# Performance work log

Hardware: AMD Instinct MI355X
Metric: run time of the kernel (lower is better)

Reference implementation:

```python
import jax, jax.numpy as jnp
import numpy as np

D_MODEL = 1024
SCALE = 1.0 / np.sqrt(D_MODEL).astype(np.float32)


def setup_inputs() -> dict:
    key = jax.random.key(0)
    ks = jax.random.split(key, 9)
    B, S, D = 4, 2048, D_MODEL
    init = 1.0 / np.sqrt(D).astype(np.float32)
    return {
        "q": jax.random.normal(ks[0], (B, S, D), jnp.float32),
        "k": jax.random.normal(ks[1], (B, S, D), jnp.float32),
        "v": jax.random.normal(ks[2], (B, S, D), jnp.float32),
        "Wq": jax.random.uniform(ks[3], (D, D), jnp.float32, -init, init),
        "bq": jax.random.uniform(ks[4], (D,), jnp.float32, -init, init),
        "Wk": jax.random.uniform(ks[5], (D, D), jnp.float32, -init, init),
        "bk": jax.random.uniform(ks[6], (D,), jnp.float32, -init, init),
        "Wv": jax.random.uniform(ks[7], (D, D), jnp.float32, -init, init),
        "bv": jax.random.uniform(ks[8], (D,), jnp.float32, -init, init),
    }


def reference(q, k, v, Wq, bq, Wk, bk, Wv, bv):
    # Linear projections (torch Linear: x @ W.T + b)
    qp = jnp.einsum('bsd,ed->bse', q, Wq) + bq
    kp = jnp.einsum('bsd,ed->bse', k, Wk) + bk
    vp = jnp.einsum('bsd,ed->bse', v, Wv) + bv
    qp = jax.nn.softmax(qp, axis=-1)          # softmax over feature dim
    kp = jax.nn.softmax(kp, axis=-2) * SCALE  # softmax over sequence dim
    vp = jax.nn.softmax(vp, axis=-2)          # softmax over sequence dim
    attn_weights = jnp.einsum('bqd,bkd->bqk', qp, kp)  # [B,S,S]
    output = jnp.einsum('bqk,bkd->bqd', attn_weights, vp)
    return (output, attn_weights)
```

## Files before the change

### kernel.cpp

```cpp
#include <hip/hip_runtime.h>
#include <math.h>


typedef float  f32x4  __attribute__((ext_vector_type(4)));
typedef __bf16 bf16x8 __attribute__((ext_vector_type(8)));
typedef int    i32x4  __attribute__((ext_vector_type(4)));
typedef unsigned short u16;

__device__ __forceinline__ float b2f(u16 u) {
    unsigned int i = ((unsigned int)u) << 16; float f;
    __builtin_memcpy(&f, &i, 4); return f;
}
__device__ __forceinline__ u16 f2b(float f) {
    unsigned int i; __builtin_memcpy(&i, &f, 4);
    i += 0x7FFFu + ((i >> 16) & 1u);
    return (u16)(i >> 16);
}

__global__ __launch_bounds__(256) void cvt_all(
    const float4* __restrict__ q, const float4* __restrict__ k,
    const float4* __restrict__ v, const float4* __restrict__ Wq,
    const float4* __restrict__ Wk, const float4* __restrict__ Wv,
    const float* __restrict__ bq, const float* __restrict__ bk,
    const float* __restrict__ bv,
    ushort4* __restrict__ qb, ushort4* __restrict__ kb,
    ushort4* __restrict__ vb, ushort4* __restrict__ Wb,
    float* __restrict__ biasCat)
{
    int bid = blockIdx.x, t = threadIdx.x;
    const float4* s; ushort4* d; int idx;
    if (bid < 8192)       { s = q;  d = qb;            idx = bid * 256 + t; }
    else if (bid < 16384) { s = k;  d = kb;            idx = (bid - 8192) * 256 + t; }
    else if (bid < 24576) { s = v;  d = vb;            idx = (bid - 16384) * 256 + t; }
    else if (bid < 25600) { s = Wq; d = Wb;            idx = (bid - 24576) * 256 + t; }
    else if (bid < 26624) { s = Wk; d = Wb + 262144;   idx = (bid - 25600) * 256 + t; }
    else if (bid < 27648) { s = Wv; d = Wb + 524288;   idx = (bid - 26624) * 256 + t; }
    else {
        for (int i = t; i < 3072; i += 256)
            biasCat[i] = (i < 1024) ? bq[i] : (i < 2048) ? bk[i - 1024] : bv[i - 2048];
        return;
    }
    float4 vv = s[idx];
    ushort4 o;
    o.x = f2b(vv.x); o.y = f2b(vv.y); o.z = f2b(vv.z); o.w = f2b(vv.w);
    d[idx] = o;
}

__global__ __launch_bounds__(512, 2) void gemm256_attn(
    const u16* __restrict__ Ap, const u16* __restrict__ Bp,
    float* __restrict__ C32, u16* __restrict__ C16,
    int N, int K, long long sA, long long sB, long long sC)
{
    __shared__ __align__(16) u16 lds[65536];

    const int tid  = threadIdx.x;
    const int lane = tid & 63;
    const int w    = tid >> 6;
    const int wr   = w >> 2, wc = w & 3;

    const int gx  = gridDim.x;
    const int tot = gx * gridDim.y;
    const int lin = blockIdx.y * gx + blockIdx.x;
    const int vlin = (lin & 7) * (tot >> 3) + (lin >> 3);
    const int bx = vlin % gx, by = vlin / gx;
    const int m0 = by * 256, n0 = bx * 256;
    const int z  = blockIdx.z;

    const u16* Ag = Ap + (size_t)z * sA;
    const u16* Bg = Bp + (size_t)z * sB;

    const int cl = tid ^ ((tid >> 4) & 6);
    const int lr = cl >> 3;
    const int ce = (cl & 7) * 8;
    const int arow = m0 + lr;
    const int brow = n0 + (lr & 31) + ((lr & 32) << 1);

    const int axr = ((lane >> 2) & 3) << 4;
    const int ar0 = (wr * 64 + (lane & 15)) * 64 + (lane >> 4) * 8;
    const int br0 = (wc * 32 + (lane & 15)) * 64 + (lane >> 4) * 8;

#define GLL16(gsrc, ldsoff)                                                    \
    __builtin_amdgcn_global_load_lds(                                          \
        (__attribute__((address_space(1))) void*)(uintptr_t)(gsrc),            \
        (__attribute__((address_space(3))) void*)&lds[ldsoff], 16, 0, 0)

#define STAGE_A(c, h, T)                                                       \
    do { const u16* _s = Ag + (size_t)(arow + (h) * 64) * K + (T) * 64 + ce;   \
         int _d = (((c) << 1) + (h)) * 8192 + tid * 8;                         \
         GLL16(_s, _d); GLL16(_s + (size_t)128 * K, _d + 4096); } while (0)

#define STAGE_B(c, g, T)                                                       \
    do { const u16* _s = Bg + (size_t)(brow + (g) * 32) * K + (T) * 64 + ce;   \
         int _d = 32768 + (((c) << 1) + (g)) * 8192 + tid * 8;                 \
         GLL16(_s, _d); GLL16(_s + (size_t)128 * K, _d + 4096); } while (0)

#define SBAR asm volatile("s_barrier" ::: "memory")

#define LDA(base)                                                              \
    _Pragma("unroll") for (int mi2 = 0; mi2 < 4; ++mi2)                        \
    _Pragma("unroll") for (int ks = 0; ks < 2; ++ks)                           \
        afr[mi2][ks] = __builtin_bit_cast(bf16x8,                              \
            *(const i32x4*)&lds[(base) + ((ar0 + mi2 * 1024 + ks * 32) ^ axr)]);

#define LDB(dst, base)                                                         \
    _Pragma("unroll") for (int ni2 = 0; ni2 < 2; ++ni2)                        \
    _Pragma("unroll") for (int ks = 0; ks < 2; ++ks)                           \
        dst[ni2][ks] = __builtin_bit_cast(bf16x8,                              \
            *(const i32x4*)&lds[(base) + ((br0 + ni2 * 1024 + ks * 32) ^ axr)]);

#define MFMA_Q(mb, nb, bfrag)                                                  \
    __builtin_amdgcn_s_setprio(1);                                             \
    _Pragma("unroll") for (int mi2 = 0; mi2 < 4; ++mi2)                        \
    _Pragma("unroll") for (int ni2 = 0; ni2 < 2; ++ni2)                        \
    _Pragma("unroll") for (int ks = 0; ks < 2; ++ks)                           \
        acc[(mb) + mi2][(nb) + ni2] = __builtin_amdgcn_mfma_f32_16x16x32_bf16( \
            afr[mi2][ks], bfrag[ni2][ks], acc[(mb) + mi2][(nb) + ni2], 0, 0, 0); \
    __builtin_amdgcn_s_setprio(0)

    f32x4 acc[8][4];
#pragma unroll
    for (int i = 0; i < 8; ++i)
#pragma unroll
        for (int j = 0; j < 4; ++j) acc[i][j] = (f32x4)0.0f;

    bf16x8 afr[4][2], b0f[2][2], b1f[2][2];

    const int nt = K >> 6;

    STAGE_A(0, 0, 0); STAGE_B(0, 0, 0);
    STAGE_A(0, 1, 0); STAGE_B(0, 1, 0);
    STAGE_A(1, 0, 1); STAGE_B(1, 0, 1);

    for (int T = 0; T < nt; ++T) {
        const int cur = T & 1, nxt = cur ^ 1;
        const int ab = (cur << 1) * 8192;
        const int bb = 32768 + (cur << 1) * 8192;

        if (T + 1 < nt) asm volatile("s_waitcnt vmcnt(4)" ::: "memory");
        else            asm volatile("s_waitcnt vmcnt(0)" ::: "memory");
        SBAR;
        LDA(ab); LDB(b0f, bb);
        if (T + 1 < nt) STAGE_B(nxt, 1, T + 1);
        SBAR;
        MFMA_Q(0, 0, b0f);
        SBAR;
        LDB(b1f, bb + 8192);
        if (T + 1 < nt) STAGE_A(nxt, 1, T + 1);
        SBAR;
        MFMA_Q(0, 2, b1f);
        SBAR;
        LDA(ab + 8192);
        if (T + 2 < nt) STAGE_A(cur, 0, T + 2);
        SBAR;
        MFMA_Q(4, 0, b0f);
        SBAR;
        if (T + 2 < nt) STAGE_B(cur, 0, T + 2);
        SBAR;
        MFMA_Q(4, 2, b1f);
        SBAR;
    }

    const int cr0 = m0 + wr * 128 + ((lane >> 4) << 2);
    const int cc0 = n0 + wc * 64 + (lane & 15);
    float* Cg = C32 + (size_t)z * sC;
#pragma unroll
    for (int mi = 0; mi < 8; ++mi)
#pragma unroll
        for (int ni = 0; ni < 4; ++ni)
#pragma unroll
            for (int j = 0; j < 4; ++j)
                Cg[(size_t)(cr0 + mi * 16 + j) * N + cc0 + ni * 16] = acc[mi][ni][j];

    u16* sE = lds;
    u16* Cb = C16 + (size_t)z * sC;
    const int wrow0 = ((lane >> 4) << 2);
    const int wcol0 = wc * 64 + (lane & 15);
    const int rr = tid >> 2;
    const int c0 = (tid & 3) * 8;
    __syncthreads();
#pragma unroll
    for (int p = 0; p < 2; ++p) {
        if (wr == p) {
#pragma unroll
            for (int mi = 0; mi < 8; ++mi)
#pragma unroll
                for (int ni = 0; ni < 4; ++ni)
#pragma unroll
                    for (int j = 0; j < 4; ++j)
                        sE[(wrow0 + mi * 16 + j) * 264 + wcol0 + ni * 16] =
                            f2b(acc[mi][ni][j]);
        }
        __syncthreads();
#pragma unroll
        for (int i = 0; i < 8; ++i) {
            i32x4 vv = *(const i32x4*)&sE[rr * 264 + c0 + i * 32];
            *(i32x4*)&Cb[(size_t)(m0 + p * 128 + rr) * N + n0 + c0 + i * 32] = vv;
        }
        if (p == 0) __syncthreads();
    }
#undef GLL16
#undef STAGE_A
#undef STAGE_B
#undef SBAR
#undef LDA
#undef LDB
#undef MFMA_Q
}

template<int EPI, int BM>
__global__ __launch_bounds__(256, BM == 128 ? 3 : 2) void gemm_bw(
    const u16* __restrict__ Ap, const u16* __restrict__ Bp,
    float* __restrict__ C32, u16* __restrict__ C16, u16* __restrict__ Calt,
    const float* __restrict__ bias, const float* __restrict__ vinv,
    int N, int K, long long sA, long long sB, long long sC)
{
    constexpr int AMI = BM / 32;
    constexpr int ALD = BM / 64;
    constexpr int ASZ = BM * 32;
    constexpr int BUF = ASZ + 4096;
    __shared__ __align__(16) u16 lds[3 * BUF];

    const int tid  = threadIdx.x;
    const int lane = tid & 63;
    const int w    = tid >> 6;
    const int wr   = w >> 1, wc = w & 1;

    const int gx  = gridDim.x;
    const int tot = gx * gridDim.y;
    const int lin = blockIdx.y * gx + blockIdx.x;
    const int vlin = (lin & 7) * (tot >> 3) + (lin >> 3);
    const int bx = vlin % gx, by = vlin / gx;
    const int m0 = by * BM, n0 = bx * 128;
    const int z  = blockIdx.z;

    const u16* Ag = Ap + (size_t)z * sA;
    const u16* Bg = Bp + (size_t)z * sB;

    const int cltid = tid ^ ((tid >> 3) & 3);
    const int crow  = cltid >> 2;
    const int ce    = (cltid & 3) * 8;

    const int exr = ((lane >> 1) & 3) << 3;
    const int ar0 = (wr * (BM / 2) + (lane & 15)) * 32 + (lane >> 4) * 8;
    const int br0 = (wc * 64 + (lane & 15)) * 32 + (lane >> 4) * 8;

#define GLLW(gsrc, ldsoff)                                                     \
    __builtin_amdgcn_global_load_lds(                                          \
        (__attribute__((address_space(1))) void*)(uintptr_t)(gsrc),            \
        (__attribute__((address_space(3))) void*)&lds[ldsoff], 16, 0, 0)

#define STAGE(buf, T)                                                          \
    do {                                                                       \
        _Pragma("unroll") for (int ld = 0; ld < ALD; ++ld)                     \
            GLLW(Ag + (size_t)(m0 + ld * 64 + crow) * K + (T) * 32 + ce,       \
                 (buf) + ld * 2048 + tid * 8);                                 \
        _Pragma("unroll") for (int ld = 0; ld < 2; ++ld)                       \
            GLLW(Bg + (size_t)(n0 + ld * 64 + crow) * K + (T) * 32 + ce,       \
                 (buf) + ASZ + ld * 2048 + tid * 8);                           \
    } while (0)

    f32x4 acc[AMI][4];
#pragma unroll
    for (int i = 0; i < AMI; ++i)
#pragma unroll
        for (int j = 0; j < 4; ++j) acc[i][j] = (f32x4)0.0f;

    bf16x8 afr[AMI], bfr[4];

    const int nt = K >> 5;

    int b0 = 0, b1 = BUF, b2 = 2 * BUF;
    STAGE(b0, 0); STAGE(b1, 1);

    for (int T = 0; T < nt; ++T) {
        if (T + 1 < nt) {
            if constexpr (BM == 256) asm volatile("s_waitcnt vmcnt(6)" ::: "memory");
            else                     asm volatile("s_waitcnt vmcnt(4)" ::: "memory");
        } else {
            asm volatile("s_waitcnt vmcnt(0)" ::: "memory");
        }
        asm volatile("s_barrier" ::: "memory");
#pragma unroll
        for (int mi = 0; mi < AMI; ++mi)
            afr[mi] = __builtin_bit_cast(bf16x8,
                *(const i32x4*)&lds[b0 + ((ar0 + mi * 512) ^ exr)]);
#pragma unroll
        for (int ni = 0; ni < 4; ++ni)
            bfr[ni] = __builtin_bit_cast(bf16x8,
                *(const i32x4*)&lds[b0 + ASZ + ((br0 + ni * 512) ^ exr)]);
        if (T + 2 < nt) STAGE(b2, T + 2);
        __builtin_amdgcn_s_setprio(1);
#pragma unroll
        for (int mi = 0; mi < AMI; ++mi)
#pragma unroll
            for (int ni = 0; ni < 4; ++ni)
                acc[mi][ni] = __builtin_amdgcn_mfma_f32_16x16x32_bf16(
                    afr[mi], bfr[ni], acc[mi][ni], 0, 0, 0);
        __builtin_amdgcn_s_setprio(0);
        int tmp = b0; b0 = b1; b1 = b2; b2 = tmp;
    }

    if constexpr (EPI == 1) {
        u16* sE = lds;
        u16* Cb = (z == 2) ? Calt : (C16 + (size_t)z * sC);
        const int colb = wc * 64 + (lane & 15);
        float bv[4];
#pragma unroll
        for (int ni = 0; ni < 4; ++ni)
            bv[ni] = bias[(size_t)z * 1024 + n0 + colb + ni * 16];
        const int wrow0 = wr * (BM / 2) + ((lane >> 4) << 2);
        __syncthreads();
#pragma unroll
        for (int mi = 0; mi < AMI; ++mi)
#pragma unroll
            for (int ni = 0; ni < 4; ++ni)
#pragma unroll
                for (int j = 0; j < 4; ++j)
                    sE[(wrow0 + mi * 16 + j) * 136 + colb + ni * 16] =
                        f2b(__expf(acc[mi][ni][j] + bv[ni]));
        __syncthreads();
        const int rr = tid >> 2, c0 = (tid & 3) * 8;
#pragma unroll
        for (int rb = 0; rb < BM / 64; ++rb) {
            int row = rb * 64 + rr;
#pragma unroll
            for (int i = 0; i < 4; ++i) {
                i32x4 vv = *(const i32x4*)&sE[row * 136 + c0 + i * 32];
                *(i32x4*)&Cb[(size_t)(m0 + row) * N + n0 + c0 + i * 32] = vv;
            }
        }
    } else {
        float* Cg = C32 + (size_t)z * sC;
        const int cr0 = m0 + wr * (BM / 2) + ((lane >> 4) << 2);
        const int cc0 = n0 + wc * 64 + (lane & 15);
        float vs[4];
#pragma unroll
        for (int ni = 0; ni < 4; ++ni)
            vs[ni] = vinv[(size_t)z * 1024 + cc0 + ni * 16];
#pragma unroll
        for (int mi = 0; mi < AMI; ++mi)
#pragma unroll
            for (int ni = 0; ni < 4; ++ni)
#pragma unroll
                for (int j = 0; j < 4; ++j)
                    Cg[(size_t)(cr0 + mi * 16 + j) * N + cc0 + ni * 16] =
                        acc[mi][ni][j] * vs[ni];
    }
#undef GLLW
#undef STAGE
}

__global__ __launch_bounds__(256) void colpart(
    const u16* __restrict__ kE, const u16* __restrict__ vE,
    float* __restrict__ kpart, float* __restrict__ vpart)
{
    int j = blockIdx.x, t = threadIdx.x;
    const u16* d; float* part;
    if (j < 64) { d = kE; part = kpart; } else { d = vE; part = vpart; j -= 64; }
    int b = j >> 4, c = j & 15;
    const u16* base = d + ((size_t)b * 2048 + c * 128) * 1024 + t * 4;
    float a0 = 0, a1 = 0, a2 = 0, a3 = 0;
    for (int s = 0; s < 128; ++s) {
        ushort4 v = *(const ushort4*)(base + (size_t)s * 1024);
        a0 += b2f(v.x); a1 += b2f(v.y); a2 += b2f(v.z); a3 += b2f(v.w);
    }
    *(float4*)(part + ((size_t)(b * 16 + c)) * 1024 + t * 4) = make_float4(a0, a1, a2, a3);
}

__global__ __launch_bounds__(256) void col_reduce2(
    const float* __restrict__ kpart, const float* __restrict__ vpart,
    float* __restrict__ kinv, float* __restrict__ vinv)
{
    int bid = blockIdx.x;
    const float* part; float* inv; float mult;
    if (bid < 16) { part = kpart; inv = kinv; mult = 0.03125f; }
    else          { part = vpart; inv = vinv; mult = 1.0f; bid -= 16; }
    int idx = bid * 256 + threadIdx.x;
    int b = idx >> 10, e = idx & 1023;
    float s = 0;
    for (int c = 0; c < 16; ++c) s += part[((size_t)(b * 16 + c)) * 1024 + e];
    inv[idx] = mult / s;
}

__global__ __launch_bounds__(256) void qsm_scale(
    u16* __restrict__ qE, const float* __restrict__ kinv)
{
    size_t row = blockIdx.x;
    int b = (int)(row >> 11);
    u16* p = qE + row * 1024;
    int t = threadIdx.x;
    ushort4 v = *(ushort4*)&p[t * 4];
    float e0 = b2f(v.x), e1 = b2f(v.y), e2 = b2f(v.z), e3 = b2f(v.w);
    float s = (e0 + e1) + (e2 + e3);
#pragma unroll
    for (int off = 32; off; off >>= 1) s += __shfl_down(s, off);
    __shared__ float red[4];
    if ((t & 63) == 0) red[t >> 6] = s;
    __syncthreads();
    float inv = 1.0f / ((red[0] + red[1]) + (red[2] + red[3]));
    float4 kv = *(const float4*)(kinv + b * 1024 + t * 4);
    ushort4 o;
    o.x = f2b(e0 * inv * kv.x); o.y = f2b(e1 * inv * kv.y);
    o.z = f2b(e2 * inv * kv.z); o.w = f2b(e3 * inv * kv.w);
    *(ushort4*)&p[t * 4] = o;
}

__global__ __launch_bounds__(256) void vtrans(
    const u16* __restrict__ vE, u16* __restrict__ vET)
{
    __shared__ __align__(16) u16 tile[64][68];
    int j = blockIdx.x, t = threadIdx.x;
    int b = j >> 9, y = (j >> 5) & 15, x = j & 31;
    int s0 = x * 64, e0 = y * 64;
    int lr = t >> 4, lc = (t & 15) * 4;
#pragma unroll
    for (int i = 0; i < 4; ++i) {
        int sr = i * 16 + lr;
        ushort4 v = *(const ushort4*)(vE + ((size_t)b * 2048 + s0 + sr) * 1024 + e0 + lc);
        tile[sr][lc] = v.x; tile[sr][lc + 1] = v.y;
        tile[sr][lc + 2] = v.z; tile[sr][lc + 3] = v.w;
    }
    __syncthreads();
#pragma unroll
    for (int i = 0; i < 4; ++i) {
        int er = i * 16 + lr;
        ushort4 v;
        v.x = tile[lc + 0][er]; v.y = tile[lc + 1][er];
        v.z = tile[lc + 2][er]; v.w = tile[lc + 3][er];
        *(ushort4*)(vET + ((size_t)b * 1024 + e0 + er) * 2048 + s0 + lc) = v;
    }
}

extern "C" void kernel_launch(void* const* d_in, const int* in_sizes, int n_in,
                              void* d_out, int out_size, void* d_ws, size_t ws_size,
                              hipStream_t stream)
{
    const float* q  = (const float*)d_in[0];
    const float* k  = (const float*)d_in[1];
    const float* v  = (const float*)d_in[2];
    const float* Wq = (const float*)d_in[3];
    const float* bq = (const float*)d_in[4];
    const float* Wk = (const float*)d_in[5];
    const float* bk = (const float*)d_in[6];
    const float* Wv = (const float*)d_in[7];
    const float* bv = (const float*)d_in[8];

    float* out  = (float*)d_out;
    float* attn = out + 8388608;

    u16* wsU = (u16*)d_ws;
    u16* qE   = wsU;
    u16* kE   = wsU + 8388608;
    u16* Wb   = wsU + 16777216;
    u16* qb   = wsU + 25165824;
    u16* kb   = wsU + 33554432;
    u16* vb   = wsU + 41943040;
    u16* vET  = wsU + 25165824;
    u16* attnB = wsU + 33554432;
    u16* vE   = (u16*)attn;

    float* tail  = (float*)(wsU + 50331648);
    float* kpart = tail;
    float* vpart = tail + 65536;
    float* kinv  = tail + 131072;
    float* vinv  = tail + 135168;
    float* biasCat = tail + 139264;

    const long long SD = 2048LL * 1024, SS = 2048LL * 2048, DS = 1024LL * 2048;

    cvt_all<<<dim3(27649), dim3(256), 0, stream>>>(
        (const float4*)q, (const float4*)k, (const float4*)v,
        (const float4*)Wq, (const float4*)Wk, (const float4*)Wv,
        bq, bk, bv,
        (ushort4*)qb, (ushort4*)kb, (ushort4*)vb, (ushort4*)Wb, biasCat);

    gemm_bw<1, 256><<<dim3(8, 32, 3), dim3(256), 0, stream>>>(
        qb, Wb, nullptr, qE, vE, biasCat, nullptr,
        1024, 1024, 8388608LL, 1048576LL, 8388608LL);

    colpart<<<dim3(128), dim3(256), 0, stream>>>(kE, vE, kpart, vpart);

    col_reduce2<<<dim3(32), dim3(256), 0, stream>>>(kpart, vpart, kinv, vinv);

    qsm_scale<<<dim3(8192), dim3(256), 0, stream>>>(qE, kinv);

    vtrans<<<dim3(2048), dim3(256), 0, stream>>>(vE, vET);

    gemm256_attn<<<dim3(8, 8, 4), dim3(512), 0, stream>>>(
        qE, kE, attn, attnB, 2048, 1024, SD, SD, SS);

    gemm_bw<2, 128><<<dim3(8, 16, 4), dim3(256), 0, stream>>>(
        attnB, vET, out, nullptr, nullptr, nullptr, vinv,
        1024, 2048, SS, DS, SD);
}
```

Measured before the change: 209.3 us.

## Fuse column sums into projection epilogue via atomics and merge qsm with vtrans

The projection GEMM epilogue now accumulates per-column sums of the exponentiated K and V tiles and adds them into a zeroed buffer with atomicAdd. This replaces the separate colpart and col_reduce2 kernels. The q row-softmax scaling and the V transpose are merged into one launch, and reciprocals are computed where they are consumed. This drops two full reads of kE and vE and three kernel launches, at the cost of atomic contention and nondeterministic summation order.

```diff
diff --git a/kernel.cpp b/kernel.cpp
--- a/kernel.cpp
+++ b/kernel.cpp
@@ -25,7 +25,7 @@
     const float* __restrict__ bv,
     ushort4* __restrict__ qb, ushort4* __restrict__ kb,
     ushort4* __restrict__ vb, ushort4* __restrict__ Wb,
-    float* __restrict__ biasCat)
+    float* __restrict__ biasCat, float* __restrict__ csum)
 {
     int bid = blockIdx.x, t = threadIdx.x;
     const float4* s; ushort4* d; int idx;
@@ -38,6 +38,7 @@
     else {
         for (int i = t; i < 3072; i += 256)
             biasCat[i] = (i < 1024) ? bq[i] : (i < 2048) ? bk[i - 1024] : bv[i - 2048];
+        for (int i = t; i < 8192; i += 256) csum[i] = 0.0f;
         return;
     }
     float4 vv = s[idx];
@@ -211,7 +212,7 @@
 __global__ __launch_bounds__(256, BM == 128 ? 3 : 2) void gemm_bw(
     const u16* __restrict__ Ap, const u16* __restrict__ Bp,
     float* __restrict__ C32, u16* __restrict__ C16, u16* __restrict__ Calt,
-    const float* __restrict__ bias, const float* __restrict__ vinv,
+    const float* __restrict__ bias, float* __restrict__ aux,
     int N, int K, long long sA, long long sB, long long sC)
 {
     constexpr int AMI = BM / 32;
@@ -304,10 +305,12 @@
         u16* sE = lds;
         u16* Cb = (z == 2) ? Calt : (C16 + (size_t)z * sC);
         const int colb = wc * 64 + (lane & 15);
-        float bv[4];
-#pragma unroll
-        for (int ni = 0; ni < 4; ++ni)
+        float bv[4], cs[4];
+#pragma unroll
+        for (int ni = 0; ni < 4; ++ni) {
             bv[ni] = bias[(size_t)z * 1024 + n0 + colb + ni * 16];
+            cs[ni] = 0.0f;
+        }
         const int wrow0 = wr * (BM / 2) + ((lane >> 4) << 2);
         __syncthreads();
 #pragma unroll
@@ -315,9 +318,21 @@
 #pragma unroll
             for (int ni = 0; ni < 4; ++ni)
 #pragma unroll
-                for (int j = 0; j < 4; ++j)
-                    sE[(wrow0 + mi * 16 + j) * 136 + colb + ni * 16] =
-                        f2b(__expf(acc[mi][ni][j] + bv[ni]));
+                for (int j = 0; j < 4; ++j) {
+                    u16 h = f2b(__expf(acc[mi][ni][j] + bv[ni]));
+                    sE[(wrow0 + mi * 16 + j) * 136 + colb + ni * 16] = h;
+                    cs[ni] += b2f(h);
+                }
+        if (z >= 1) {
+            float* dst = aux + (z - 1) * 4096 + (m0 >> 11) * 1024;
+#pragma unroll
+            for (int ni = 0; ni < 4; ++ni) {
+                float s = cs[ni];
+                s += __shfl_xor(s, 16);
+                s += __shfl_xor(s, 32);
+                if (lane < 16) atomicAdd(&dst[n0 + colb + ni * 16], s);
+            }
+        }
         __syncthreads();
         const int rr = tid >> 2, c0 = (tid & 3) * 8;
 #pragma unroll
@@ -336,7 +351,7 @@
         float vs[4];
 #pragma unroll
         for (int ni = 0; ni < 4; ++ni)
-            vs[ni] = vinv[(size_t)z * 1024 + cc0 + ni * 16];
+            vs[ni] = 1.0f / aux[(size_t)z * 1024 + cc0 + ni * 16];
 #pragma unroll
         for (int mi = 0; mi < AMI; ++mi)
 #pragma unroll
@@ -350,84 +365,52 @@
 #undef STAGE
 }
 
-__global__ __launch_bounds__(256) void colpart(
-    const u16* __restrict__ kE, const u16* __restrict__ vE,
-    float* __restrict__ kpart, float* __restrict__ vpart)
-{
-    int j = blockIdx.x, t = threadIdx.x;
-    const u16* d; float* part;
-    if (j < 64) { d = kE; part = kpart; } else { d = vE; part = vpart; j -= 64; }
-    int b = j >> 4, c = j & 15;
-    const u16* base = d + ((size_t)b * 2048 + c * 128) * 1024 + t * 4;
-    float a0 = 0, a1 = 0, a2 = 0, a3 = 0;
-    for (int s = 0; s < 128; ++s) {
-        ushort4 v = *(const ushort4*)(base + (size_t)s * 1024);
-        a0 += b2f(v.x); a1 += b2f(v.y); a2 += b2f(v.z); a3 += b2f(v.w);
-    }
-    *(float4*)(part + ((size_t)(b * 16 + c)) * 1024 + t * 4) = make_float4(a0, a1, a2, a3);
-}
-
-__global__ __launch_bounds__(256) void col_reduce2(
-    const float* __restrict__ kpart, const float* __restrict__ vpart,
-    float* __restrict__ kinv, float* __restrict__ vinv)
-{
-    int bid = blockIdx.x;
-    const float* part; float* inv; float mult;
-    if (bid < 16) { part = kpart; inv = kinv; mult = 0.03125f; }
-    else          { part = vpart; inv = vinv; mult = 1.0f; bid -= 16; }
-    int idx = bid * 256 + threadIdx.x;
-    int b = idx >> 10, e = idx & 1023;
-    float s = 0;
-    for (int c = 0; c < 16; ++c) s += part[((size_t)(b * 16 + c)) * 1024 + e];
-    inv[idx] = mult / s;
-}
-
-__global__ __launch_bounds__(256) void qsm_scale(
-    u16* __restrict__ qE, const float* __restrict__ kinv)
-{
-    size_t row = blockIdx.x;
-    int b = (int)(row >> 11);
-    u16* p = qE + row * 1024;
-    int t = threadIdx.x;
-    ushort4 v = *(ushort4*)&p[t * 4];
-    float e0 = b2f(v.x), e1 = b2f(v.y), e2 = b2f(v.z), e3 = b2f(v.w);
-    float s = (e0 + e1) + (e2 + e3);
-#pragma unroll
-    for (int off = 32; off; off >>= 1) s += __shfl_down(s, off);
-    __shared__ float red[4];
-    if ((t & 63) == 0) red[t >> 6] = s;
-    __syncthreads();
-    float inv = 1.0f / ((red[0] + red[1]) + (red[2] + red[3]));
-    float4 kv = *(const float4*)(kinv + b * 1024 + t * 4);
-    ushort4 o;
-    o.x = f2b(e0 * inv * kv.x); o.y = f2b(e1 * inv * kv.y);
-    o.z = f2b(e2 * inv * kv.z); o.w = f2b(e3 * inv * kv.w);
-    *(ushort4*)&p[t * 4] = o;
-}
-
-__global__ __launch_bounds__(256) void vtrans(
+__global__ __launch_bounds__(256) void qsm_vtrans(
+    u16* __restrict__ qE, const float* __restrict__ csum,
     const u16* __restrict__ vE, u16* __restrict__ vET)
 {
     __shared__ __align__(16) u16 tile[64][68];
-    int j = blockIdx.x, t = threadIdx.x;
-    int b = j >> 9, y = (j >> 5) & 15, x = j & 31;
-    int s0 = x * 64, e0 = y * 64;
-    int lr = t >> 4, lc = (t & 15) * 4;
-#pragma unroll
-    for (int i = 0; i < 4; ++i) {
-        int sr = i * 16 + lr;
-        ushort4 v = *(const ushort4*)(vE + ((size_t)b * 2048 + s0 + sr) * 1024 + e0 + lc);
-        tile[sr][lc] = v.x; tile[sr][lc + 1] = v.y;
-        tile[sr][lc + 2] = v.z; tile[sr][lc + 3] = v.w;
-    }
-    __syncthreads();
-#pragma unroll
-    for (int i = 0; i < 4; ++i) {
-        int er = i * 16 + lr;
-        ushort4 v;
-        v.x = tile[lc + 0][er]; v.y = tile[lc + 1][er];
-        v.z = tile[lc + 2][er]; v.w = tile[lc + 3][er];
-        *(ushort4*)(vET + ((size_t)b * 1024 + e0 + er) * 2048 + s0 + lc) = v;
+    __shared__ float red[4];
+    int bid = blockIdx.x, t = threadIdx.x;
+    if (bid < 8192) {
+        int b = bid >> 11;
+        u16* p = qE + (size_t)bid * 1024;
+        ushort4 v = *(ushort4*)&p[t * 4];
+        float e0 = b2f(v.x), e1 = b2f(v.y), e2 = b2f(v.z), e3 = b2f(v.w);
+        float s = (e0 + e1) + (e2 + e3);
+#pragma unroll
+        for (int off = 32; off; off >>= 1) s += __shfl_down(s, off);
+        if ((t & 63) == 0) red[t >> 6] = s;
+        __syncthreads();
+        float inv = 1.0f / ((red[0] + red[1]) + (red[2] + red[3]));
+        float4 ks = *(const float4*)(csum + b * 1024 + t * 4);
+        float i0 = 0.03125f / ks.x, i1 = 0.03125f / ks.y;
+        float i2 = 0.03125f / ks.z, i3 = 0.03125f / ks.w;
+        ushort4 o;
+        o.x = f2b(e0 * inv * i0); o.y = f2b(e1 * inv * i1);
+        o.z = f2b(e2 * inv * i2); o.w = f2b(e3 * inv * i3);
+        *(ushort4*)&p[t * 4] = o;
+    } else {
+        int j = bid - 8192;
+        int b = j >> 9, y = (j >> 5) & 15, x = j & 31;
+        int s0 = x * 64, e0 = y * 64;
+        int lr = t >> 4, lc = (t & 15) * 4;
+#pragma unroll
+        for (int i = 0; i < 4; ++i) {
+            int sr = i * 16 + lr;
+            ushort4 v = *(const ushort4*)(vE + ((size_t)b * 2048 + s0 + sr) * 1024 + e0 + lc);
+            tile[sr][lc] = v.x; tile[sr][lc + 1] = v.y;
+            tile[sr][lc + 2] = v.z; tile[sr][lc + 3] = v.w;
+        }
+        __syncthreads();
+#pragma unroll
+        for (int i = 0; i < 4; ++i) {
+            int er = i * 16 + lr;
+            ushort4 v;
+            v.x = tile[lc + 0][er]; v.y = tile[lc + 1][er];
+            v.z = tile[lc + 2][er]; v.w = tile[lc + 3][er];
+            *(ushort4*)(vET + ((size_t)b * 1024 + e0 + er) * 2048 + s0 + lc) = v;
+        }
     }
 }
 
@@ -460,10 +443,7 @@
     u16* vE   = (u16*)attn;
 
     float* tail  = (float*)(wsU + 50331648);
-    float* kpart = tail;
-    float* vpart = tail + 65536;
-    float* kinv  = tail + 131072;
-    float* vinv  = tail + 135168;
+    float* csum  = tail;
     float* biasCat = tail + 139264;
 
     const long long SD = 2048LL * 1024, SS = 2048LL * 2048, DS = 1024LL * 2048;
@@ -472,24 +452,18 @@
         (const float4*)q, (const float4*)k, (const float4*)v,
         (const float4*)Wq, (const float4*)Wk, (const float4*)Wv,
         bq, bk, bv,
-        (ushort4*)qb, (ushort4*)kb, (ushort4*)vb, (ushort4*)Wb, biasCat);
+        (ushort4*)qb, (ushort4*)kb, (ushort4*)vb, (ushort4*)Wb, biasCat, csum);
 
     gemm_bw<1, 256><<<dim3(8, 32, 3), dim3(256), 0, stream>>>(
-        qb, Wb, nullptr, qE, vE, biasCat, nullptr,
+        qb, Wb, nullptr, qE, vE, biasCat, csum,
         1024, 1024, 8388608LL, 1048576LL, 8388608LL);
 
-    colpart<<<dim3(128), dim3(256), 0, stream>>>(kE, vE, kpart, vpart);
-
-    col_reduce2<<<dim3(32), dim3(256), 0, stream>>>(kpart, vpart, kinv, vinv);
-
-    qsm_scale<<<dim3(8192), dim3(256), 0, stream>>>(qE, kinv);
-
-    vtrans<<<dim3(2048), dim3(256), 0, stream>>>(vE, vET);
+    qsm_vtrans<<<dim3(10240), dim3(256), 0, stream>>>(qE, csum, vE, vET);
 
     gemm256_attn<<<dim3(8, 8, 4), dim3(512), 0, stream>>>(
         qE, kE, attn, attnB, 2048, 1024, SD, SD, SS);
 
     gemm_bw<2, 128><<<dim3(8, 16, 4), dim3(256), 0, stream>>>(
-        attnB, vET, out, nullptr, nullptr, nullptr, vinv,
+        attnB, vET, out, nullptr, nullptr, nullptr, csum + 4096,
         1024, 2048, SS, DS, SD);
 }
```

Result: faster. 200.4 us, median of 2 (-4.2%).
